# Kernel tuning notes

Hardware: AMD Instinct MI355X
Metric: run time of the kernel (lower is better)

## Reference

```python
import jax, jax.numpy as jnp
import numpy as np

D_MODEL = 512
NUM_HEADS = 8


def setup_inputs() -> dict:
    key = jax.random.key(0)
    ks = jax.random.split(key, 6)
    B, T, D = 4, 2048, D_MODEL
    x = jax.random.normal(ks[0], (B, T, D), dtype=jnp.float32)
    periods = jax.random.randint(ks[1], (B, NUM_HEADS), 0, 48)
    # nn.MultiheadAttention parameters: packed qkv in-projection + out-projection
    in_proj_w = jax.random.normal(ks[2], (3 * D, D), dtype=jnp.float32) * 0.02
    in_proj_b = jax.random.normal(ks[3], (3 * D,), dtype=jnp.float32) * 0.02
    out_w = jax.random.normal(ks[4], (D, D), dtype=jnp.float32) * 0.02
    out_b = jax.random.normal(ks[5], (D,), dtype=jnp.float32) * 0.02
    return {"x": x, "periods": periods, "in_proj_w": in_proj_w,
            "in_proj_b": in_proj_b, "out_w": out_w, "out_b": out_b}


def reference(x, periods, in_proj_w, in_proj_b, out_w, out_b):
    B, T, D = x.shape
    H = periods.shape[1]          # one head per period (num_heads == top_k)
    hd = D // H
    # packed qkv projection (matches torch in_proj_weight layout)
    qkv = x @ in_proj_w.T + in_proj_b            # (B,T,3D)
    q, k, v = jnp.split(qkv, 3, axis=-1)
    def to_heads(t):
        return t.reshape(B, T, H, hd).transpose(0, 2, 1, 3)  # (B,H,T,hd)
    q, k, v = to_heads(q), to_heads(k), to_heads(v)
    scores = jnp.einsum('bhqd,bhkd->bhqk', q, k) / jnp.sqrt(jnp.asarray(hd, x.dtype))
    # periodic causal mask: allow j<=i with (i-j) % P == 0
    i = jnp.arange(T)[:, None]
    j = jnp.arange(T)[None, :]
    p = jnp.maximum(periods, 1)[:, :, None, None]            # (B,H,1,1)
    allow = (j <= i) & (((i - j) % p) == 0)                  # (B,H,T,T)
    scores = jnp.where(allow, scores, -jnp.inf)              # diagonal always allowed -> no all-masked rows
    attn = jax.nn.softmax(scores, axis=-1)
    out = jnp.einsum('bhqk,bhkd->bhqd', attn, v)             # (B,H,T,hd)
    out = out.transpose(0, 2, 1, 3).reshape(B, T, D)
    return out @ out_w.T + out_b
```

## Files before the change

kernel.cpp:

```cpp
#include <hip/hip_runtime.h>
#include <math.h>

#define D_MODEL 512
#define NHEAD   8
#define HD      64
#define T_SEQ   2048
#define BATCH   4
#define M_ROWS  (BATCH * T_SEQ)

typedef __attribute__((ext_vector_type(8))) short        short8;
typedef __attribute__((ext_vector_type(4))) float        floatx4;
typedef __attribute__((ext_vector_type(4))) unsigned int uintx4;

__device__ __forceinline__ unsigned short f2bf(float f) {
    unsigned int u = __float_as_uint(f);
    unsigned int r = u + 0x7FFFu + ((u >> 16) & 1u);
    return (unsigned short)(r >> 16);
}

__device__ __forceinline__ float bf2f(unsigned short u) {
    return __uint_as_float((unsigned int)u << 16);
}

__device__ __forceinline__ float exp2_raw(float x) {
    float r;
    asm("v_exp_f32 %0, %1" : "=v"(r) : "v"(x));
    return r;
}

__device__ __forceinline__ int4 cvt8(float4 a, float4 b) {
    union { unsigned short u[8]; int4 v; } r;
    r.u[0] = f2bf(a.x); r.u[1] = f2bf(a.y); r.u[2] = f2bf(a.z); r.u[3] = f2bf(a.w);
    r.u[4] = f2bf(b.x); r.u[5] = f2bf(b.y); r.u[6] = f2bf(b.z); r.u[7] = f2bf(b.w);
    return r.v;
}

__device__ __forceinline__ void gload16(const void* g, void* l) {
    __builtin_amdgcn_global_load_lds(
        (const __attribute__((address_space(1))) void*)g,
        (__attribute__((address_space(3))) void*)l, 16, 0, 0);
}

__device__ __forceinline__ bool slot_decode(int t, int P, int& r, int& mt, int& Lr)
{
    const int q0 = T_SEQ / P, rem = T_SEQ % P;
    const int nt_hi = (q0 + 64) >> 6;
    const int nt_lo = (q0 + 63) >> 6;
    const int hi_total = rem * nt_hi;
    if (t < hi_total) {
        r = t / nt_hi; mt = t - r * nt_hi; Lr = q0 + 1;
    } else {
        t -= hi_total;
        if (t >= (P - rem) * nt_lo) return false;
        const int rr = t / nt_lo;
        r = rem + rr; mt = t - rr * nt_lo; Lr = q0;
    }
    return true;
}

#define XGROUPS  (M_ROWS * D_MODEL / 8)
#define W1GROUPS (3 * D_MODEL * D_MODEL / 8)
#define W2GROUPS (D_MODEL * D_MODEL / 8)
#define CVT_GROUPS (XGROUPS + W1GROUPS + W2GROUPS)
#define MAX_ITEMS 2560

__global__ __launch_bounds__(256) void cvt_inputs(
    const float* __restrict__ x, const float* __restrict__ w1,
    const float* __restrict__ w2, unsigned short* __restrict__ xo,
    unsigned short* __restrict__ w1o, unsigned short* __restrict__ w2o,
    const int* __restrict__ periods, int* __restrict__ items)
{
    {
        int i = blockIdx.x * 256 + threadIdx.x;
        const float* src; unsigned short* dst;
        if (i < XGROUPS)                  { src = x;  dst = xo;  }
        else if (i < XGROUPS + W1GROUPS)  { src = w1; dst = w1o; i -= XGROUPS; }
        else                              { src = w2; dst = w2o; i -= XGROUPS + W1GROUPS; }
        const float4* p = (const float4*)(src + (size_t)i * 8);
        float4 a = p[0], b = p[1];
        *(int4*)(dst + (size_t)i * 8) = cvt8(a, b);
    }
    if (blockIdx.x < 32) {
        const int bh = blockIdx.x;
        int P = periods[bh]; if (P < 1) P = 1;
        const int tid  = threadIdx.x;
        const int wave = tid >> 6, lane = tid & 63;
        const int t = 63 - (tid >> 2);
        const int c = 3 - (tid & 3);
        int r, mt, Lr;
        const bool valid = slot_decode(t, P, r, mt, Lr) && ((c << 3) <= mt);
        const unsigned long long mask = __ballot(valid);
        const int prefix = __popcll(mask & ((1ull << lane) - 1ull));
        __shared__ int wb[4];
        if (lane == 0) wb[wave] = __popcll(mask);
        if (tid < 80) items[bh * 80 + tid] = -1;
        __syncthreads();
        int base = 0;
        if (wave > 0) base += wb[0];
        if (wave > 1) base += wb[1];
        if (wave > 2) base += wb[2];
        if (valid) {
            const int rank = base + prefix;
            items[bh * 80 + ((rank + bh) % 80)] = (bh << 8) | (t << 2) | c;
        }
    }
}

__global__ __launch_bounds__(256) void qkv_gemm_mfma(
    const unsigned short* __restrict__ X,
    const unsigned short* __restrict__ W,
    const float* __restrict__ bias,
    unsigned short* __restrict__ qo, unsigned short* __restrict__ ko,
    unsigned short* __restrict__ vo)
{
    __shared__ unsigned short smem[128 * 128];
    unsigned short* const As = smem;
    unsigned short* const Bs = smem + 128 * 64;

    const int bid  = blockIdx.x;
    const int xcd  = bid & 7;
    const int chk_ = bid >> 3;
    const int row0 = (((chk_ / 12) << 3) + xcd) << 7;
    const int col0 = (chk_ % 12) << 7;

    const int tid  = threadIdx.x;
    const int wave = tid >> 6, lane = tid & 63;
    const int quad = lane >> 4, l15 = lane & 15;
    const int wm   = wave >> 1, wn = wave & 1;
    const int lr8  = lane >> 3;
    const int sc   = lane & 7;

    floatx4 acc[4][4] = {};

    for (int k0 = 0; k0 < D_MODEL; k0 += 64) {
#pragma unroll
        for (int i = 0; i < 4; ++i) {
            const int rb  = (wave << 5) + (i << 3);
            const int r   = rb + lr8;
            const int csw = sc ^ (r & 7);
            gload16(X + (size_t)(row0 + r) * D_MODEL + k0 + (csw << 3),
                    As + (rb << 6));
            gload16(W + (size_t)(col0 + r) * D_MODEL + k0 + (csw << 3),
                    Bs + (rb << 6));
        }
        __syncthreads();

#pragma unroll
        for (int ks = 0; ks < 2; ++ks) {
            short8 af[4], bfr[4];
            const int ch = (ks << 2) + quad;
#pragma unroll
            for (int mt = 0; mt < 4; ++mt) {
                const int row = (wm << 6) + (mt << 4) + l15;
                af[mt] = *(const short8*)(As + (row << 6) + ((ch ^ (row & 7)) << 3));
            }
#pragma unroll
            for (int nt = 0; nt < 4; ++nt) {
                const int col = (wn << 6) + (nt << 4) + l15;
                bfr[nt] = *(const short8*)(Bs + (col << 6) + ((ch ^ (col & 7)) << 3));
            }
#pragma unroll
            for (int mt = 0; mt < 4; ++mt)
#pragma unroll
                for (int nt = 0; nt < 4; ++nt)
                    acc[mt][nt] = __builtin_amdgcn_mfma_f32_16x16x32_bf16(
                        af[mt], bfr[nt], acc[mt][nt], 0, 0, 0);
        }
        __syncthreads();
    }

#pragma unroll
    for (int nt = 0; nt < 4; ++nt) {
        const int ncol = (wn << 6) + (nt << 4) + l15;
        const float bn = bias[col0 + ncol];
#pragma unroll
        for (int mt = 0; mt < 4; ++mt)
#pragma unroll
            for (int reg = 0; reg < 4; ++reg) {
                const int mrow = (wm << 6) + (mt << 4) + (quad << 2) + reg;
                smem[(mrow << 7) + ncol] = f2bf(acc[mt][nt][reg] + bn);
            }
    }
    __syncthreads();
    {
        const int c16  = lane & 15;
        const int rsub = lane >> 4;
        const int n0   = col0 + (c16 << 3);
        const int part = n0 >> 9;
        unsigned short* dst = (part == 0) ? qo : ((part == 1) ? ko : vo);
        const int head = (n0 & 511) >> 6, d0 = n0 & 63;
#pragma unroll
        for (int p = 0; p < 8; ++p) {
            const int ml = (wave << 5) + (p << 2) + rsub;
            const int m  = row0 + ml;
            const int b = m >> 11, t = m & 2047;
            int4 val = *(const int4*)(smem + (ml << 7) + (c16 << 3));
            *(int4*)(dst + ((((size_t)b << 3) + head) * T_SEQ + t) * HD + d0) = val;
        }
    }
}

#define SCALE2 0.18033688011112042f

__global__ __launch_bounds__(256) void attn_rc_mfma(
    const unsigned short* __restrict__ q, const unsigned short* __restrict__ k,
    const unsigned short* __restrict__ v, const int* __restrict__ periods,
    unsigned short* __restrict__ o,
    unsigned short* __restrict__ Opart, float* __restrict__ Lpart,
    const int* __restrict__ items)
{
    const int idx = items[blockIdx.x];
    if (idx < 0) return;

    __shared__ unsigned short Ks[2][64 * 64];
    __shared__ unsigned short Vt[2][64 * 64];
    __shared__ unsigned short Ps[64 * 64];

    const int bh     = idx >> 8;
    const int t_orig = (idx >> 2) & 63;
    const int c      = idx & 3;
    int P = periods[bh]; if (P < 1) P = 1;
    int r, mt, Lr;
    if (!slot_decode(t_orig, P, r, mt, Lr)) return;
    const int nch  = (mt >> 3) + 1;
    const int kt0  = c << 3;
    const int kend = (kt0 + 7 < mt) ? (kt0 + 7) : mt;
    const int m0   = mt << 6;

    const int tid  = threadIdx.x;
    const int wave = tid >> 6, lane = tid & 63;
    const int quad = lane >> 4, l15 = lane & 15;
    const int vkp  = tid & 31, vhg = tid >> 5;
    const int cpos = ((vkp >> 4) << 4) + (((vkp & 7) >> 1) << 2)
                   + (((vkp >> 3) & 1) << 1) + (vkp & 1);
    const int cgrp = cpos >> 2, clo = (cpos & 3) << 2;

    const unsigned short* hq = q + (size_t)bh * T_SEQ * HD;
    const unsigned short* hk = k + (size_t)bh * T_SEQ * HD;
    const unsigned short* hv = v + (size_t)bh * T_SEQ * HD;

    {
        const int km0 = kt0 << 6;
#pragma unroll
        for (int i = 0; i < 2; ++i) {
            const int rb  = (wave << 4) + (i << 3);
            const int rr  = rb + (lane >> 3);
            const int csw = ((lane & 7) ^ (rr & 7)) << 3;
            int mq = m0 + rr;  if (mq > Lr - 1) mq = Lr - 1;
            int mk = km0 + rr; if (mk > Lr - 1) mk = Lr - 1;
            gload16(hq + (size_t)(r + mq * P) * HD + csw, Ps + (rb << 6));
            gload16(hk + (size_t)(r + mk * P) * HD + csw, Ks[0] + (rb << 6));
        }
        int mv0 = km0 + (vkp << 1);     if (mv0 > Lr - 1) mv0 = Lr - 1;
        int mv1 = km0 + (vkp << 1) + 1; if (mv1 > Lr - 1) mv1 = Lr - 1;
        int4 va = *(const int4*)(hv + (size_t)(r + mv0 * P) * HD + (vhg << 3));
        int4 vb = *(const int4*)(hv + (size_t)(r + mv1 * P) * HD + (vhg << 3));
        const unsigned short* pa = (const unsigned short*)&va;
        const unsigned short* pb = (const unsigned short*)&vb;
#pragma unroll
        for (int j = 0; j < 8; ++j) {
            const int hd_ = (vhg << 3) + j;
            const unsigned int pk =
                (unsigned int)pa[j] | ((unsigned int)pb[j] << 16);
            *(unsigned int*)((char*)Vt[0] + (hd_ << 7) +
                             ((cgrp ^ (hd_ & 7)) << 4) + clo) = pk;
        }
    }
    __syncthreads();
    short8 qf[2];
#pragma unroll
    for (int ks = 0; ks < 2; ++ks) {
        const int row = (wave << 4) + l15;
        qf[ks] = *(const short8*)(Ps + (row << 6) +
                                  ((((ks << 2) + quad) ^ (row & 7)) << 3));
    }

    floatx4 Oa[4] = {};
    float Lacc = 0.f;
    const int qrel = (wave << 4) + l15;

    for (int kt = kt0; kt <= kend; ++kt) {
        const int buf = (kt - kt0) & 1;
        const bool havenext = kt < kend;

        int4 va, vb;
        if (havenext) {
            const int km0 = (kt + 1) << 6;
#pragma unroll
            for (int i = 0; i < 2; ++i) {
                const int rb  = (wave << 4) + (i << 3);
                const int rr  = rb + (lane >> 3);
                int mk = km0 + rr; if (mk > Lr - 1) mk = Lr - 1;
                gload16(hk + (size_t)(r + mk * P) * HD +
                            (((lane & 7) ^ (rr & 7)) << 3),
                        Ks[buf ^ 1] + (rb << 6));
            }
            int mv0 = km0 + (vkp << 1);     if (mv0 > Lr - 1) mv0 = Lr - 1;
            int mv1 = km0 + (vkp << 1) + 1; if (mv1 > Lr - 1) mv1 = Lr - 1;
            va = *(const int4*)(hv + (size_t)(r + mv0 * P) * HD + (vhg << 3));
            vb = *(const int4*)(hv + (size_t)(r + mv1 * P) * HD + (vhg << 3));
        }

        floatx4 sacc[4] = {};
        __builtin_amdgcn_s_setprio(1);
#pragma unroll
        for (int nt = 0; nt < 4; ++nt) {
            const int row = (nt << 4) + l15;
#pragma unroll
            for (int ks = 0; ks < 2; ++ks) {
                short8 kf = *(const short8*)(Ks[buf] + (row << 6) +
                                             ((((ks << 2) + quad) ^ (row & 7)) << 3));
                sacc[nt] = __builtin_amdgcn_mfma_f32_16x16x32_bf16(
                    kf, qf[ks], sacc[nt], 0, 0, 0);
            }
        }
        __builtin_amdgcn_s_setprio(0);

        const bool diag = (kt == mt);
        unsigned int wv[8];
        float rs = 0.f;
#pragma unroll
        for (int nt = 0; nt < 4; ++nt) {
            unsigned short bq[4];
#pragma unroll
            for (int reg = 0; reg < 4; ++reg) {
                const int krel = (nt << 4) + (quad << 2) + reg;
                float sv = fmaf(sacc[nt][reg], SCALE2, -8.f);
                if (diag && krel > qrel) sv = -1e30f;
                bq[reg] = f2bf(exp2_raw(sv));
                rs += bf2f(bq[reg]);
            }
            wv[(nt << 1)]     = (unsigned int)bq[0] | ((unsigned int)bq[1] << 16);
            wv[(nt << 1) | 1] = (unsigned int)bq[2] | ((unsigned int)bq[3] << 16);
        }
        Lacc += rs;
        uintx4 wA = {wv[0], wv[1], wv[2], wv[3]};
        uintx4 wB = {wv[4], wv[5], wv[6], wv[7]};
        const short8 pa0 = __builtin_bit_cast(short8, wA);
        const short8 pa1 = __builtin_bit_cast(short8, wB);

        __builtin_amdgcn_s_setprio(1);
#pragma unroll
        for (int nt = 0; nt < 4; ++nt) {
            const int row = (nt << 4) + l15;
#pragma unroll
            for (int ks = 0; ks < 2; ++ks) {
                short8 vf = *(const short8*)(Vt[buf] + (row << 6) +
                                             ((((ks << 2) + quad) ^ (row & 7)) << 3));
                Oa[nt] = __builtin_amdgcn_mfma_f32_16x16x32_bf16(
                    ks ? pa1 : pa0, vf, Oa[nt], 0, 0, 0);
            }
        }
        __builtin_amdgcn_s_setprio(0);

        if (havenext) {
            const unsigned short* pa = (const unsigned short*)&va;
            const unsigned short* pb = (const unsigned short*)&vb;
#pragma unroll
            for (int j = 0; j < 8; ++j) {
                const int hd_ = (vhg << 3) + j;
                const unsigned int pk =
                    (unsigned int)pa[j] | ((unsigned int)pb[j] << 16);
                *(unsigned int*)((char*)Vt[buf ^ 1] + (hd_ << 7) +
                                 ((cgrp ^ (hd_ & 7)) << 4) + clo) = pk;
            }
        }
        __syncthreads();
    }

    Lacc += __shfl_xor(Lacc, 16);
    Lacc += __shfl_xor(Lacc, 32);
    float l_i[4];
#pragma unroll
    for (int reg = 0; reg < 4; ++reg)
        l_i[reg] = __shfl(Lacc, (lane & 48) | (quad << 2) | reg);

    if (nch == 1) {
#pragma unroll
        for (int reg = 0; reg < 4; ++reg) {
            const float invl = 1.f / l_i[reg];
            const int row = (wave << 4) + (quad << 2) + reg;
#pragma unroll
            for (int nt = 0; nt < 4; ++nt)
                Ks[0][(row << 6) + (nt << 4) + l15] = f2bf(Oa[nt][reg] * invl);
        }
        const int lrow = lane >> 2;
        const int chk  = (lane & 3) << 1;
        const int ml   = (wave << 4) + lrow;
        const int m    = m0 + ml;
        if (m < Lr) {
            const size_t base = ((size_t)bh * T_SEQ + (r + m * P)) * HD;
            int4 w0 = *(const int4*)(Ks[0] + (ml << 6) + (chk << 3));
            int4 w1 = *(const int4*)(Ks[0] + (ml << 6) + ((chk + 1) << 3));
            *(int4*)(o + base + (chk << 3))       = w0;
            *(int4*)(o + base + ((chk + 1) << 3)) = w1;
        }
    } else {
        const size_t slot = ((size_t)((bh << 6) + t_orig) << 2) + c;
#pragma unroll
        for (int reg = 0; reg < 4; ++reg) {
            const int row = (wave << 4) + (quad << 2) + reg;
#pragma unroll
            for (int nt = 0; nt < 4; ++nt)
                Ks[0][(row << 6) + (nt << 4) + l15] = f2bf(Oa[nt][reg]);
            if (l15 == 0)
                Lpart[slot * 64 + row] = l_i[reg];
        }
        const int lrow = lane >> 2;
        const int chk  = (lane & 3) << 1;
        const int ml   = (wave << 4) + lrow;
        unsigned short* dst = Opart + slot * 4096 + (ml << 6);
        *(int4*)(dst + (chk << 3))       = *(const int4*)(Ks[0] + (ml << 6) + (chk << 3));
        *(int4*)(dst + ((chk + 1) << 3)) = *(const int4*)(Ks[0] + (ml << 6) + ((chk + 1) << 3));
    }
}

__global__ __launch_bounds__(256) void reduce_rc(
    const int* __restrict__ periods,
    const unsigned short* __restrict__ Opart, const float* __restrict__ Lpart,
    unsigned short* __restrict__ o)
{
    const int bh = blockIdx.y;
    int P = periods[bh]; if (P < 1) P = 1;
    const int t = blockIdx.x;
    int r, mt, Lr;
    if (!slot_decode(t, P, r, mt, Lr)) return;
    const int nch = (mt >> 3) + 1;
    if (nch < 2) return;

    const int tid = threadIdx.x;
    const int row = tid >> 2;
    const int cg  = (tid & 3) << 4;
    const int m   = (mt << 6) + row;
    if (m >= Lr) return;

    const size_t slot0 = (size_t)((bh << 6) + t) << 2;

    float lsum = 0.f;
    for (int cc = 0; cc < nch; ++cc)
        lsum += Lpart[(slot0 + cc) * 64 + row];
    const float inv = 1.f / lsum;

    float ov[16] = {};
    for (int cc = 0; cc < nch; ++cc) {
        const unsigned short* p = Opart + (slot0 + cc) * 4096 + (row << 6) + cg;
#pragma unroll
        for (int j = 0; j < 16; ++j) ov[j] += bf2f(p[j]);
    }
    unsigned short outv[16];
#pragma unroll
    for (int j = 0; j < 16; ++j) outv[j] = f2bf(ov[j] * inv);

    unsigned short* dst = o + ((size_t)bh * T_SEQ + (r + m * P)) * HD + cg;
    *(int4*)dst       = *(const int4*)&outv[0];
    *(int4*)(dst + 8) = *(const int4*)&outv[8];
}

__global__ __launch_bounds__(256) void out_gemm_mfma(
    const unsigned short* __restrict__ A,
    const unsigned short* __restrict__ W,
    const float* __restrict__ bias,
    float* __restrict__ out)
{
    __shared__ unsigned short As[64 * 64];
    __shared__ unsigned short Bs[128 * 64];

    const int tid  = threadIdx.x;
    const int wave = tid >> 6, lane = tid & 63;
    const int quad = lane >> 4, l15 = lane & 15;
    const int wm   = wave >> 1, wn = wave & 1;
    const int row0 = blockIdx.x * 64;
    const int col0 = blockIdx.y * 128;
    const int lr8  = lane >> 3;
    const int sc   = lane & 7;

    floatx4 acc[2][4] = {};

    for (int k0 = 0; k0 < D_MODEL; k0 += 64) {
        const int h = k0 >> 6;
#pragma unroll
        for (int i = 0; i < 4; ++i) {
            const int rb  = (wave << 5) + (i << 3);
            const int r   = rb + lr8;
            const int csw = sc ^ (r & 7);
            gload16(W + (size_t)(col0 + r) * D_MODEL + k0 + (csw << 3),
                    Bs + (rb << 6));
        }
#pragma unroll
        for (int i = 0; i < 2; ++i) {
            const int rb  = (wave << 4) + (i << 3);
            const int r   = rb + lr8;
            const int csw = sc ^ (r & 7);
            const int rg = row0 + r;
            const int b = rg >> 11, t = rg & 2047;
            gload16(A + ((((size_t)b << 3) + h) * T_SEQ + t) * HD + (csw << 3),
                    As + (rb << 6));
        }
        __syncthreads();

#pragma unroll
        for (int ks = 0; ks < 2; ++ks) {
            short8 af[2], bfr[4];
            const int ch = (ks << 2) + quad;
#pragma unroll
            for (int mt = 0; mt < 2; ++mt) {
                const int row = (wm << 5) + (mt << 4) + l15;
                af[mt] = *(const short8*)(As + (row << 6) + ((ch ^ (row & 7)) << 3));
            }
#pragma unroll
            for (int nt = 0; nt < 4; ++nt) {
                const int col = (wn << 6) + (nt << 4) + l15;
                bfr[nt] = *(const short8*)(Bs + (col << 6) + ((ch ^ (col & 7)) << 3));
            }
#pragma unroll
            for (int mt = 0; mt < 2; ++mt)
#pragma unroll
                for (int nt = 0; nt < 4; ++nt)
                    acc[mt][nt] = __builtin_amdgcn_mfma_f32_16x16x32_bf16(
                        af[mt], bfr[nt], acc[mt][nt], 0, 0, 0);
        }
        __syncthreads();
    }

#pragma unroll
    for (int nt = 0; nt < 4; ++nt) {
        const int n = col0 + (wn << 6) + (nt << 4) + l15;
        const float bn = bias[n];
#pragma unroll
        for (int mt = 0; mt < 2; ++mt) {
#pragma unroll
            for (int reg = 0; reg < 4; ++reg) {
                const int m = row0 + (wm << 5) + (mt << 4) + (quad << 2) + reg;
                out[(size_t)m * D_MODEL + n] = acc[mt][nt][reg] + bn;
            }
        }
    }
}

extern "C" void kernel_launch(void* const* d_in, const int* in_sizes, int n_in,
                              void* d_out, int out_size, void* d_ws, size_t ws_size,
                              hipStream_t stream)
{
    const float* x        = (const float*)d_in[0];
    const int*   periods  = (const int*)  d_in[1];
    const float* in_w     = (const float*)d_in[2];
    const float* in_b     = (const float*)d_in[3];
    const float* out_w    = (const float*)d_in[4];
    const float* out_b    = (const float*)d_in[5];
    float*       out      = (float*)d_out;

    const size_t TENS = (size_t)BATCH * NHEAD * T_SEQ * HD;
    unsigned short* qb    = (unsigned short*)d_ws;
    unsigned short* kb    = qb + TENS;
    unsigned short* vb    = kb + TENS;
    unsigned short* aob   = vb + TENS;
    unsigned short* Opart = aob + TENS;
    float*          Lpart = (float*)(Opart + (size_t)8192 * 4096);
    unsigned short* Xb    = (unsigned short*)(Lpart + (size_t)8192 * 64);
    unsigned short* W1b   = Xb + (size_t)M_ROWS * D_MODEL;
    unsigned short* W2b   = W1b + (size_t)3 * D_MODEL * D_MODEL;
    int*            items = (int*)(W2b + (size_t)D_MODEL * D_MODEL);

    cvt_inputs<<<CVT_GROUPS / 256, 256, 0, stream>>>(x, in_w, out_w,
                                                     Xb, W1b, W2b,
                                                     periods, items);

    qkv_gemm_mfma<<<(M_ROWS / 128) * ((3 * D_MODEL) / 128), 256, 0, stream>>>(
        Xb, W1b, in_b, qb, kb, vb);

    attn_rc_mfma<<<MAX_ITEMS, 256, 0, stream>>>(qb, kb, vb, periods, aob,
                                                Opart, Lpart, items);
    reduce_rc<<<dim3(64, BATCH * NHEAD), 256, 0, stream>>>(
        periods, Opart, Lpart, aob);

    dim3 g3(M_ROWS / 64, D_MODEL / 128);
    out_gemm_mfma<<<g3, 256, 0, stream>>>(aob, W2b, out_b, out);
}
```

Before: 134.8 us.

## Fuse split-K reduction into attention kernel via last-block atomic counter

Measured after the change: 141.5 us. +5.0%, slower.

```diff
diff --git a/kernel.cpp b/kernel.cpp
--- a/kernel.cpp
+++ b/kernel.cpp
@@ -68,7 +68,8 @@
     const float* __restrict__ x, const float* __restrict__ w1,
     const float* __restrict__ w2, unsigned short* __restrict__ xo,
     unsigned short* __restrict__ w1o, unsigned short* __restrict__ w2o,
-    const int* __restrict__ periods, int* __restrict__ items)
+    const int* __restrict__ periods, int* __restrict__ items,
+    int* __restrict__ ncnt)
 {
     {
         int i = blockIdx.x * 256 + threadIdx.x;
@@ -94,6 +95,7 @@
         __shared__ int wb[4];
         if (lane == 0) wb[wave] = __popcll(mask);
         if (tid < 80) items[bh * 80 + tid] = -1;
+        if (tid < 64) ncnt[(bh << 6) + tid] = 0;
         __syncthreads();
         int base = 0;
         if (wave > 0) base += wb[0];
@@ -207,14 +209,13 @@
     const unsigned short* __restrict__ v, const int* __restrict__ periods,
     unsigned short* __restrict__ o,
     unsigned short* __restrict__ Opart, float* __restrict__ Lpart,
-    const int* __restrict__ items)
+    const int* __restrict__ items, int* __restrict__ ncnt)
 {
     const int idx = items[blockIdx.x];
     if (idx < 0) return;
 
     __shared__ unsigned short Ks[2][64 * 64];
     __shared__ unsigned short Vt[2][64 * 64];
-    __shared__ unsigned short Ps[64 * 64];
 
     const int bh     = idx >> 8;
     const int t_orig = (idx >> 2) & 63;
@@ -248,7 +249,7 @@
             const int csw = ((lane & 7) ^ (rr & 7)) << 3;
             int mq = m0 + rr;  if (mq > Lr - 1) mq = Lr - 1;
             int mk = km0 + rr; if (mk > Lr - 1) mk = Lr - 1;
-            gload16(hq + (size_t)(r + mq * P) * HD + csw, Ps + (rb << 6));
+            gload16(hq + (size_t)(r + mq * P) * HD + csw, Ks[1] + (rb << 6));
             gload16(hk + (size_t)(r + mk * P) * HD + csw, Ks[0] + (rb << 6));
         }
         int mv0 = km0 + (vkp << 1);     if (mv0 > Lr - 1) mv0 = Lr - 1;
@@ -271,9 +272,10 @@
 #pragma unroll
     for (int ks = 0; ks < 2; ++ks) {
         const int row = (wave << 4) + l15;
-        qf[ks] = *(const short8*)(Ps + (row << 6) +
+        qf[ks] = *(const short8*)(Ks[1] + (row << 6) +
                                   ((((ks << 2) + quad) ^ (row & 7)) << 3));
     }
+    __syncthreads();
 
     floatx4 Oa[4] = {};
     float Lacc = 0.f;
@@ -396,7 +398,8 @@
             *(int4*)(o + base + ((chk + 1) << 3)) = w1;
         }
     } else {
-        const size_t slot = ((size_t)((bh << 6) + t_orig) << 2) + c;
+        const int  slot_id = (bh << 6) + t_orig;
+        const size_t slot0 = (size_t)slot_id << 2;
 #pragma unroll
         for (int reg = 0; reg < 4; ++reg) {
             const int row = (wave << 4) + (quad << 2) + reg;
@@ -404,56 +407,48 @@
             for (int nt = 0; nt < 4; ++nt)
                 Ks[0][(row << 6) + (nt << 4) + l15] = f2bf(Oa[nt][reg]);
             if (l15 == 0)
-                Lpart[slot * 64 + row] = l_i[reg];
-        }
-        const int lrow = lane >> 2;
-        const int chk  = (lane & 3) << 1;
-        const int ml   = (wave << 4) + lrow;
-        unsigned short* dst = Opart + slot * 4096 + (ml << 6);
-        *(int4*)(dst + (chk << 3))       = *(const int4*)(Ks[0] + (ml << 6) + (chk << 3));
-        *(int4*)(dst + ((chk + 1) << 3)) = *(const int4*)(Ks[0] + (ml << 6) + ((chk + 1) << 3));
-    }
-}
-
-__global__ __launch_bounds__(256) void reduce_rc(
-    const int* __restrict__ periods,
-    const unsigned short* __restrict__ Opart, const float* __restrict__ Lpart,
-    unsigned short* __restrict__ o)
-{
-    const int bh = blockIdx.y;
-    int P = periods[bh]; if (P < 1) P = 1;
-    const int t = blockIdx.x;
-    int r, mt, Lr;
-    if (!slot_decode(t, P, r, mt, Lr)) return;
-    const int nch = (mt >> 3) + 1;
-    if (nch < 2) return;
-
-    const int tid = threadIdx.x;
-    const int row = tid >> 2;
-    const int cg  = (tid & 3) << 4;
-    const int m   = (mt << 6) + row;
-    if (m >= Lr) return;
-
-    const size_t slot0 = (size_t)((bh << 6) + t) << 2;
-
-    float lsum = 0.f;
-    for (int cc = 0; cc < nch; ++cc)
-        lsum += Lpart[(slot0 + cc) * 64 + row];
-    const float inv = 1.f / lsum;
-
-    float ov[16] = {};
-    for (int cc = 0; cc < nch; ++cc) {
-        const unsigned short* p = Opart + (slot0 + cc) * 4096 + (row << 6) + cg;
-#pragma unroll
-        for (int j = 0; j < 16; ++j) ov[j] += bf2f(p[j]);
-    }
-    unsigned short outv[16];
-#pragma unroll
-    for (int j = 0; j < 16; ++j) outv[j] = f2bf(ov[j] * inv);
-
-    unsigned short* dst = o + ((size_t)bh * T_SEQ + (r + m * P)) * HD + cg;
-    *(int4*)dst       = *(const int4*)&outv[0];
-    *(int4*)(dst + 8) = *(const int4*)&outv[8];
+                Lpart[(slot0 + c) * 64 + row] = l_i[reg];
+        }
+        {
+            const int lrow = lane >> 2;
+            const int chk  = (lane & 3) << 1;
+            const int ml   = (wave << 4) + lrow;
+            unsigned short* dst = Opart + (slot0 + c) * 4096 + (ml << 6);
+            *(int4*)(dst + (chk << 3))       = *(const int4*)(Ks[0] + (ml << 6) + (chk << 3));
+            *(int4*)(dst + ((chk + 1) << 3)) = *(const int4*)(Ks[0] + (ml << 6) + ((chk + 1) << 3));
+        }
+        __threadfence();
+        __syncthreads();
+        int* flag = (int*)&Vt[1][0];
+        if (tid == 0) *flag = atomicAdd(&ncnt[slot_id], 1);
+        __syncthreads();
+        if (*flag == nch - 1) {
+            __threadfence();
+            const int row = tid >> 2;
+            const int cg  = (tid & 3) << 4;
+            const int m   = m0 + row;
+            if (m < Lr) {
+                float lsum = 0.f;
+                for (int cc = 0; cc < nch; ++cc)
+                    lsum += Lpart[(slot0 + cc) * 64 + row];
+                const float inv = 1.f / lsum;
+                float ov[16] = {};
+                for (int cc = 0; cc < nch; ++cc) {
+                    const unsigned short* p =
+                        Opart + (slot0 + cc) * 4096 + (row << 6) + cg;
+#pragma unroll
+                    for (int j = 0; j < 16; ++j) ov[j] += bf2f(p[j]);
+                }
+                unsigned short outv[16];
+#pragma unroll
+                for (int j = 0; j < 16; ++j) outv[j] = f2bf(ov[j] * inv);
+                unsigned short* dst =
+                    o + ((size_t)bh * T_SEQ + (r + m * P)) * HD + cg;
+                *(int4*)dst       = *(const int4*)&outv[0];
+                *(int4*)(dst + 8) = *(const int4*)&outv[8];
+            }
+        }
+    }
 }
 
 __global__ __launch_bounds__(256) void out_gemm_mfma(
@@ -560,18 +555,17 @@
     unsigned short* W1b   = Xb + (size_t)M_ROWS * D_MODEL;
     unsigned short* W2b   = W1b + (size_t)3 * D_MODEL * D_MODEL;
     int*            items = (int*)(W2b + (size_t)D_MODEL * D_MODEL);
+    int*            ncnt  = items + MAX_ITEMS;
 
     cvt_inputs<<<CVT_GROUPS / 256, 256, 0, stream>>>(x, in_w, out_w,
                                                      Xb, W1b, W2b,
-                                                     periods, items);
+                                                     periods, items, ncnt);
 
     qkv_gemm_mfma<<<(M_ROWS / 128) * ((3 * D_MODEL) / 128), 256, 0, stream>>>(
         Xb, W1b, in_b, qb, kb, vb);
 
     attn_rc_mfma<<<MAX_ITEMS, 256, 0, stream>>>(qb, kb, vb, periods, aob,
-                                                Opart, Lpart, items);
-    reduce_rc<<<dim3(64, BATCH * NHEAD), 256, 0, stream>>>(
-        periods, Opart, Lpart, aob);
+                                                Opart, Lpart, items, ncnt);
 
     dim3 g3(M_ROWS / 64, D_MODEL / 128);
     out_gemm_mfma<<<g3, 256, 0, stream>>>(aob, W2b, out_b, out);
```
